# Optimization experiments

Measured on AMD Instinct MI355X. Metric: run time of the kernel, lower is better.

Reference implementation:

```python
import jax, jax.numpy as jnp
import numpy as np

B, N_IN, N_HID, T = 64, 512, 512, 512


def setup_inputs() -> dict:
    key = jax.random.key(0)
    k1, k2, k3, k4, k5 = jax.random.split(key, 5)
    scale = 1.0 / np.sqrt(N_HID).astype(np.float32)
    return {
        "X": jax.random.normal(k1, (B, N_IN, T), dtype=jnp.float32),
        "Wax": jax.random.normal(k2, (N_IN, N_HID), dtype=jnp.float32) * scale,
        "Waa": jax.random.normal(k3, (N_HID, N_HID), dtype=jnp.float32) * scale,
        "bx": jax.random.normal(k4, (N_HID,), dtype=jnp.float32) * scale,
        "ba": jax.random.normal(k5, (N_HID,), dtype=jnp.float32) * scale,
    }


def reference(X, Wax, Waa, bx, ba):
    # X: [B, n_in, T]. a_{t+1} = tanh(x_t @ Wax + bx + a_t @ Waa + ba)
    # Precompute the input projections for all timesteps in one big GEMM:
    # [T, B, n_hid]
    Xt = jnp.transpose(X, (2, 0, 1))  # [T, B, n_in]
    inp_proj = jnp.einsum('tbi,ih->tbh', Xt, Wax) + bx + ba

    def step(a, u):
        a_next = jnp.tanh(u + a @ Waa)
        return a_next, a_next

    a0 = jnp.zeros((X.shape[0], Waa.shape[0]), dtype=X.dtype)
    _, A = jax.lax.scan(step, a0, inp_proj)
    return A  # [T, B, n_hid] == stacked A[1:] of the torch module
```

## Files before the change

kernel.cpp:

```cpp
#include <hip/hip_runtime.h>
#include <math.h>

#define BB   64
#define NIN  512
#define NH   512
#define TT   512

typedef _Float16 half2_t __attribute__((ext_vector_type(2)));
typedef _Float16 half8_t __attribute__((ext_vector_type(8)));
typedef float    f32x4  __attribute__((ext_vector_type(4)));

__device__ __forceinline__ unsigned pk16(float x, float y) {
    unsigned lo = (unsigned)__builtin_bit_cast(unsigned short, (_Float16)x);
    unsigned hi = (unsigned)__builtin_bit_cast(unsigned short, (_Float16)y);
    return lo | (hi << 16);
}

__device__ __forceinline__ float dot2u(unsigned w, unsigned a, float acc) {
    return __builtin_amdgcn_fdot2(__builtin_bit_cast(half2_t, w),
                                  __builtin_bit_cast(half2_t, a), acc, false);
}

__device__ __forceinline__ float tanh_fast(float x) {
    float ax = __builtin_fabsf(x);
    float e  = __builtin_amdgcn_exp2f(-2.885390082f * ax);
    float r  = (1.0f - e) * __builtin_amdgcn_rcpf(1.0f + e);
    return __builtin_copysignf(r, x);
}

#define NX4 (BB * (NIN / 2) * (TT / 4))
#define NW4 ((NIN / 2) * (NH / 4))

__global__ __launch_bounds__(256) void pack_f16(
    const float* __restrict__ X, const float* __restrict__ Wax,
    unsigned* __restrict__ Xp, unsigned* __restrict__ Wp)
{
    const int gid = blockIdx.x * 256 + threadIdx.x;
    if (gid < NX4) {
        const int t4 = gid & (TT / 4 - 1);
        const int pr = gid >> 7;
        const int j  = pr & (NIN / 2 - 1);
        const int b  = pr >> 8;
        float4 r0 = *(const float4*)&X[((size_t)b * NIN + 2 * j    ) * TT + t4 * 4];
        float4 r1 = *(const float4*)&X[((size_t)b * NIN + 2 * j + 1) * TT + t4 * 4];
        uint4 o;
        o.x = pk16(r0.x, r1.x); o.y = pk16(r0.y, r1.y);
        o.z = pk16(r0.z, r1.z); o.w = pk16(r0.w, r1.w);
        *(uint4*)&Xp[(size_t)pr * TT + t4 * 4] = o;
    } else {
        const int g = gid - NX4;
        if (g < NW4) {
            const int h4 = g & (NH / 4 - 1);
            const int j  = g >> 7;
            float4 r0 = *(const float4*)&Wax[((size_t)(2 * j    )) * NH + h4 * 4];
            float4 r1 = *(const float4*)&Wax[((size_t)(2 * j + 1)) * NH + h4 * 4];
            uint4 o;
            o.x = pk16(r0.x, r1.x); o.y = pk16(r0.y, r1.y);
            o.z = pk16(r0.z, r1.z); o.w = pk16(r0.w, r1.w);
            *(uint4*)&Wp[(size_t)j * NH + h4 * 4] = o;
        }
    }
}

__global__ __launch_bounds__(256) void inp_proj_mfma_pk(
    const unsigned* __restrict__ Xp, const unsigned* __restrict__ Wp,
    const float* __restrict__ bx, const float* __restrict__ ba,
    float* __restrict__ out)
{
    __shared__ unsigned Xsp[16][132];
    __shared__ unsigned Wsp[16][132];

    const int b   = blockIdx.z;
    const int t0  = blockIdx.y * 128;
    const int h0  = blockIdx.x * 128;
    const int tid = threadIdx.x;
    const int lane = tid & 63;
    const int wid  = tid >> 6;
    const int wm   = wid >> 1;
    const int wn   = wid & 1;
    const int q    = lane >> 4;
    const int r16  = lane & 15;

    const int lr = tid >> 4;
    const int lc = (tid & 15) * 8;

    const unsigned* Xb = Xp + (size_t)b * (NIN / 2) * TT;

    f32x4 acc[4][4] = {};

    for (int p0 = 0; p0 < NIN / 2; p0 += 16) {
        const unsigned* Arow = &Xb[(size_t)(p0 + lr) * TT + t0 + lc];
        const unsigned* Brow = &Wp[(size_t)(p0 + lr) * NH + h0 + lc];
        uint4 xa = *(const uint4*)&Arow[0];
        uint4 xb = *(const uint4*)&Arow[4];
        uint4 wa = *(const uint4*)&Brow[0];
        uint4 wb = *(const uint4*)&Brow[4];

        __syncthreads();
        *(uint4*)&Xsp[lr][lc]     = xa;
        *(uint4*)&Xsp[lr][lc + 4] = xb;
        *(uint4*)&Wsp[lr][lc]     = wa;
        *(uint4*)&Wsp[lr][lc + 4] = wb;
        __syncthreads();

        uint4 af[4], bf[4];
#pragma unroll
        for (int mt = 0; mt < 4; ++mt) {
            const int tc = wm * 64 + mt * 16 + r16;
            af[mt].x = Xsp[4 * q + 0][tc];
            af[mt].y = Xsp[4 * q + 1][tc];
            af[mt].z = Xsp[4 * q + 2][tc];
            af[mt].w = Xsp[4 * q + 3][tc];
        }
#pragma unroll
        for (int nt = 0; nt < 4; ++nt) {
            const int hc = wn * 64 + nt * 16 + r16;
            bf[nt].x = Wsp[4 * q + 0][hc];
            bf[nt].y = Wsp[4 * q + 1][hc];
            bf[nt].z = Wsp[4 * q + 2][hc];
            bf[nt].w = Wsp[4 * q + 3][hc];
        }
#pragma unroll
        for (int mt = 0; mt < 4; ++mt)
#pragma unroll
            for (int nt = 0; nt < 4; ++nt)
                acc[mt][nt] = __builtin_amdgcn_mfma_f32_16x16x32_f16(
                    __builtin_bit_cast(half8_t, af[mt]),
                    __builtin_bit_cast(half8_t, bf[nt]),
                    acc[mt][nt], 0, 0, 0);
    }

#pragma unroll
    for (int nt = 0; nt < 4; ++nt) {
        const int h = h0 + wn * 64 + nt * 16 + r16;
        const float bias = bx[h] + ba[h];
#pragma unroll
        for (int mt = 0; mt < 4; ++mt) {
            const int trow = t0 + wm * 64 + mt * 16 + q * 4;
#pragma unroll
            for (int rr = 0; rr < 4; ++rr) {
                out[(size_t)(trow + rr) * (BB * NH) + (size_t)b * NH + h] =
                    acc[mt][nt][rr] + bias;
            }
        }
    }
}

__global__ __launch_bounds__(256) void inp_proj_mfma(
    const float* __restrict__ X, const float* __restrict__ Wax,
    const float* __restrict__ bx, const float* __restrict__ ba,
    float* __restrict__ out)
{
    __shared__ unsigned Xsp[16][132];
    __shared__ unsigned Wsp[16][132];

    const int b   = blockIdx.z;
    const int t0  = blockIdx.y * 128;
    const int h0  = blockIdx.x * 128;
    const int tid = threadIdx.x;
    const int lane = tid & 63;
    const int wid  = tid >> 6;
    const int wm   = wid >> 1;
    const int wn   = wid & 1;
    const int q    = lane >> 4;
    const int r16  = lane & 15;

    const int lr = tid >> 4;
    const int lc = (tid & 15) * 8;

    const float* Xb = X + (size_t)b * NIN * TT;

    f32x4 acc[4][4] = {};

    for (int i0 = 0; i0 < NIN; i0 += 32) {
        const int k0 = i0 + 2 * lr, k1 = k0 + 1;
        float4 xa0 = *(const float4*)&Xb[(size_t)k0 * TT + t0 + lc];
        float4 xa1 = *(const float4*)&Xb[(size_t)k0 * TT + t0 + lc + 4];
        float4 xb0 = *(const float4*)&Xb[(size_t)k1 * TT + t0 + lc];
        float4 xb1 = *(const float4*)&Xb[(size_t)k1 * TT + t0 + lc + 4];
        float4 wa0 = *(const float4*)&Wax[(size_t)k0 * NH + h0 + lc];
        float4 wa1 = *(const float4*)&Wax[(size_t)k0 * NH + h0 + lc + 4];
        float4 wb0 = *(const float4*)&Wax[(size_t)k1 * NH + h0 + lc];
        float4 wb1 = *(const float4*)&Wax[(size_t)k1 * NH + h0 + lc + 4];

        uint4 xp0, xp1, wp0, wp1;
        xp0.x = pk16(xa0.x, xb0.x); xp0.y = pk16(xa0.y, xb0.y);
        xp0.z = pk16(xa0.z, xb0.z); xp0.w = pk16(xa0.w, xb0.w);
        xp1.x = pk16(xa1.x, xb1.x); xp1.y = pk16(xa1.y, xb1.y);
        xp1.z = pk16(xa1.z, xb1.z); xp1.w = pk16(xa1.w, xb1.w);
        wp0.x = pk16(wa0.x, wb0.x); wp0.y = pk16(wa0.y, wb0.y);
        wp0.z = pk16(wa0.z, wb0.z); wp0.w = pk16(wa0.w, wb0.w);
        wp1.x = pk16(wa1.x, wb1.x); wp1.y = pk16(wa1.y, wb1.y);
        wp1.z = pk16(wa1.z, wb1.z); wp1.w = pk16(wa1.w, wb1.w);

        __syncthreads();
        *(uint4*)&Xsp[lr][lc]     = xp0;
        *(uint4*)&Xsp[lr][lc + 4] = xp1;
        *(uint4*)&Wsp[lr][lc]     = wp0;
        *(uint4*)&Wsp[lr][lc + 4] = wp1;
        __syncthreads();

        uint4 af[4], bf[4];
#pragma unroll
        for (int mt = 0; mt < 4; ++mt) {
            const int tc = wm * 64 + mt * 16 + r16;
            af[mt].x = Xsp[4 * q + 0][tc];
            af[mt].y = Xsp[4 * q + 1][tc];
            af[mt].z = Xsp[4 * q + 2][tc];
            af[mt].w = Xsp[4 * q + 3][tc];
        }
#pragma unroll
        for (int nt = 0; nt < 4; ++nt) {
            const int hc = wn * 64 + nt * 16 + r16;
            bf[nt].x = Wsp[4 * q + 0][hc];
            bf[nt].y = Wsp[4 * q + 1][hc];
            bf[nt].z = Wsp[4 * q + 2][hc];
            bf[nt].w = Wsp[4 * q + 3][hc];
        }
#pragma unroll
        for (int mt = 0; mt < 4; ++mt)
#pragma unroll
            for (int nt = 0; nt < 4; ++nt)
                acc[mt][nt] = __builtin_amdgcn_mfma_f32_16x16x32_f16(
                    __builtin_bit_cast(half8_t, af[mt]),
                    __builtin_bit_cast(half8_t, bf[nt]),
                    acc[mt][nt], 0, 0, 0);
    }

#pragma unroll
    for (int nt = 0; nt < 4; ++nt) {
        const int h = h0 + wn * 64 + nt * 16 + r16;
        const float bias = bx[h] + ba[h];
#pragma unroll
        for (int mt = 0; mt < 4; ++mt) {
            const int trow = t0 + wm * 64 + mt * 16 + q * 4;
#pragma unroll
            for (int rr = 0; rr < 4; ++rr) {
                out[(size_t)(trow + rr) * (BB * NH) + (size_t)b * NH + h] =
                    acc[mt][nt][rr] + bias;
            }
        }
    }
}

#define NRP 24
#define NLP 8
#define PSTRIDE 516

__device__ __forceinline__ unsigned bline(unsigned a, int l) {
    return (unsigned)__builtin_amdgcn_readlane((int)a, l);
}

__global__ __launch_bounds__(1024, 4) void rnn_scan_v6(
    const float* __restrict__ Waa, float* __restrict__ out)
{
    __shared__ uint4    wldsv[NLP][1024];
    __shared__ unsigned a_lds[2][256];
    __shared__ float    part[8][PSTRIDE];

    const int tid  = threadIdx.x;
    const int b    = blockIdx.x;
    const int cidx = tid & 127;
    const int kq   = tid >> 7;
    const int h4   = cidx * 4;
    const int l32  = tid & 31;

    unsigned w0[NRP], w1[NRP], w2[NRP], w3[NRP];
#pragma unroll
    for (int j = 0; j < NRP; ++j) {
        const int k = kq * 64 + 2 * j;
        float4 r0 = *(const float4*)&Waa[(size_t)k       * NH + h4];
        float4 r1 = *(const float4*)&Waa[(size_t)(k + 1) * NH + h4];
        w0[j] = pk16(r0.x, r1.x);
        w1[j] = pk16(r0.y, r1.y);
        w2[j] = pk16(r0.z, r1.z);
        w3[j] = pk16(r0.w, r1.w);
    }
#pragma unroll
    for (int p = 0; p < NLP; ++p) {
        const int k = kq * 64 + 2 * (NRP + p);
        float4 r0 = *(const float4*)&Waa[(size_t)k       * NH + h4];
        float4 r1 = *(const float4*)&Waa[(size_t)(k + 1) * NH + h4];
        uint4 wv;
        wv.x = pk16(r0.x, r1.x);
        wv.y = pk16(r0.y, r1.y);
        wv.z = pk16(r0.z, r1.z);
        wv.w = pk16(r0.w, r1.w);
        wldsv[p][tid] = wv;
    }

    if (tid < 256) a_lds[0][tid] = 0u;
    __syncthreads();

    const int  hc  = tid & 511;
    const bool red = (tid < 512);
    float* ob = out + (size_t)b * NH + hc;
    float u_cur = red ? ob[0] : 0.0f;

    for (int t = 0; t < TT; ++t) {
        const int tn = (t + 1 < TT) ? (t + 1) : (TT - 1);
        float u_next = red ? ob[(size_t)tn * (BB * NH)] : 0.0f;

        unsigned a_loc = a_lds[t & 1][kq * 32 + l32];

        float acc0 = 0.f, acc1 = 0.f, acc2 = 0.f, acc3 = 0.f;
#pragma unroll
        for (int j = 0; j < NRP; j += 2) {
            unsigned ra = bline(a_loc, j);
            unsigned rb = bline(a_loc, j + 1);
            acc0 = dot2u(w0[j], ra, acc0);
            acc1 = dot2u(w1[j], ra, acc1);
            acc2 = dot2u(w2[j], ra, acc2);
            acc3 = dot2u(w3[j], ra, acc3);
            acc0 = dot2u(w0[j + 1], rb, acc0);
            acc1 = dot2u(w1[j + 1], rb, acc1);
            acc2 = dot2u(w2[j + 1], rb, acc2);
            acc3 = dot2u(w3[j + 1], rb, acc3);
        }
#pragma unroll
        for (int p = 0; p < NLP; ++p) {
            unsigned ra = bline(a_loc, NRP + p);
            uint4 v = wldsv[p][tid];
            acc0 = dot2u(v.x, ra, acc0);
            acc1 = dot2u(v.y, ra, acc1);
            acc2 = dot2u(v.z, ra, acc2);
            acc3 = dot2u(v.w, ra, acc3);
        }

        float4 pv; pv.x = acc0; pv.y = acc1; pv.z = acc2; pv.w = acc3;
        *(float4*)&part[kq][h4] = pv;
        __builtin_amdgcn_s_waitcnt(0xC07F);
        __builtin_amdgcn_s_barrier();

        if (red) {
            float x = u_cur +
                (((part[0][hc] + part[1][hc]) + (part[2][hc] + part[3][hc])) +
                 ((part[4][hc] + part[5][hc]) + (part[6][hc] + part[7][hc])));
            float an = tanh_fast(x);
            ob[(size_t)t * (BB * NH)] = an;
            ((unsigned short*)a_lds[(t + 1) & 1])[hc] =
                __builtin_bit_cast(unsigned short, (_Float16)an);
        }
        u_cur = u_next;
        __builtin_amdgcn_s_waitcnt(0xC07F);
        __builtin_amdgcn_s_barrier();
    }
}

extern "C" void kernel_launch(void* const* d_in, const int* in_sizes, int n_in,
                              void* d_out, int out_size, void* d_ws, size_t ws_size,
                              hipStream_t stream) {
    const float* X   = (const float*)d_in[0];
    const float* Wax = (const float*)d_in[1];
    const float* Waa = (const float*)d_in[2];
    const float* bx  = (const float*)d_in[3];
    const float* ba  = (const float*)d_in[4];
    float* out = (float*)d_out;

    const size_t xp_dw = (size_t)BB * (NIN / 2) * TT;
    const size_t wp_dw = (size_t)(NIN / 2) * NH;
    const size_t need  = (xp_dw + wp_dw) * sizeof(unsigned);

    if (ws_size >= need) {
        unsigned* Xp = (unsigned*)d_ws;
        unsigned* Wp = Xp + xp_dw;
        const int npack = (NX4 + NW4 + 255) / 256;
        pack_f16<<<npack, 256, 0, stream>>>(X, Wax, Xp, Wp);
        dim3 g1(NH / 128, TT / 128, BB);
        inp_proj_mfma_pk<<<g1, 256, 0, stream>>>(Xp, Wp, bx, ba, out);
    } else {
        dim3 g1(NH / 128, TT / 128, BB);
        inp_proj_mfma<<<g1, 256, 0, stream>>>(X, Wax, bx, ba, out);
    }
    rnn_scan_v6<<<BB, 1024, 0, stream>>>(Waa, out);
}
```

Baseline: 965.2 us.

## Reduce RNN step partials via LDS atomics and drop second barrier

```diff
diff --git a/kernel.cpp b/kernel.cpp
--- a/kernel.cpp
+++ b/kernel.cpp
@@ -245,63 +245,65 @@
 
 #define NRP 24
 #define NLP 8
-#define PSTRIDE 516
 
 __device__ __forceinline__ unsigned bline(unsigned a, int l) {
     return (unsigned)__builtin_amdgcn_readlane((int)a, l);
 }
 
-__global__ __launch_bounds__(1024, 4) void rnn_scan_v6(
+__global__ __launch_bounds__(1024, 4) void rnn_scan_v8(
     const float* __restrict__ Waa, float* __restrict__ out)
 {
-    __shared__ uint4    wldsv[NLP][1024];
-    __shared__ unsigned a_lds[2][256];
-    __shared__ float    part[8][PSTRIDE];
+    __shared__ uint4 wldsv[NLP][1024];
+    __shared__ float part[3][512];
 
     const int tid  = threadIdx.x;
     const int b    = blockIdx.x;
     const int cidx = tid & 127;
     const int kq   = tid >> 7;
-    const int h4   = cidx * 4;
     const int l32  = tid & 31;
+    const int wv   = tid >> 6;
 
     unsigned w0[NRP], w1[NRP], w2[NRP], w3[NRP];
 #pragma unroll
     for (int j = 0; j < NRP; ++j) {
         const int k = kq * 64 + 2 * j;
-        float4 r0 = *(const float4*)&Waa[(size_t)k       * NH + h4];
-        float4 r1 = *(const float4*)&Waa[(size_t)(k + 1) * NH + h4];
-        w0[j] = pk16(r0.x, r1.x);
-        w1[j] = pk16(r0.y, r1.y);
-        w2[j] = pk16(r0.z, r1.z);
-        w3[j] = pk16(r0.w, r1.w);
+        const float* r0 = &Waa[(size_t)k * NH + cidx];
+        const float* r1 = &Waa[(size_t)(k + 1) * NH + cidx];
+        w0[j] = pk16(r0[0],   r1[0]);
+        w1[j] = pk16(r0[128], r1[128]);
+        w2[j] = pk16(r0[256], r1[256]);
+        w3[j] = pk16(r0[384], r1[384]);
     }
 #pragma unroll
     for (int p = 0; p < NLP; ++p) {
         const int k = kq * 64 + 2 * (NRP + p);
-        float4 r0 = *(const float4*)&Waa[(size_t)k       * NH + h4];
-        float4 r1 = *(const float4*)&Waa[(size_t)(k + 1) * NH + h4];
-        uint4 wv;
-        wv.x = pk16(r0.x, r1.x);
-        wv.y = pk16(r0.y, r1.y);
-        wv.z = pk16(r0.z, r1.z);
-        wv.w = pk16(r0.w, r1.w);
-        wldsv[p][tid] = wv;
-    }
-
-    if (tid < 256) a_lds[0][tid] = 0u;
+        const float* r0 = &Waa[(size_t)k * NH + cidx];
+        const float* r1 = &Waa[(size_t)(k + 1) * NH + cidx];
+        uint4 wvv;
+        wvv.x = pk16(r0[0],   r1[0]);
+        wvv.y = pk16(r0[128], r1[128]);
+        wvv.z = pk16(r0[256], r1[256]);
+        wvv.w = pk16(r0[384], r1[384]);
+        wldsv[p][tid] = wvv;
+    }
+
+    if (tid < 512) {
+        part[0][tid] = 0.0f;
+        part[1][tid] = 0.0f;
+        part[2][tid] = 0.0f;
+    }
     __syncthreads();
 
-    const int  hc  = tid & 511;
-    const bool red = (tid < 512);
-    float* ob = out + (size_t)b * NH + hc;
-    float u_cur = red ? ob[0] : 0.0f;
-
+    const int h2 = kq * 64 + 2 * l32;
+    const float* ub = out + (size_t)b * NH + h2;
+    float2 u_cur = *(const float2*)ub;
+    unsigned a_loc = 0u;
+    const bool gate = ((tid & 32) == 0) && ((wv & 1) == 0);
+
+    int pb = 0;
     for (int t = 0; t < TT; ++t) {
         const int tn = (t + 1 < TT) ? (t + 1) : (TT - 1);
-        float u_next = red ? ob[(size_t)tn * (BB * NH)] : 0.0f;
-
-        unsigned a_loc = a_lds[t & 1][kq * 32 + l32];
+        float2 u_next = *(const float2*)&ub[(size_t)tn * (BB * NH)];
 
         float acc0 = 0.f, acc1 = 0.f, acc2 = 0.f, acc3 = 0.f;
 #pragma unroll
@@ -327,23 +329,28 @@
             acc3 = dot2u(v.w, ra, acc3);
         }
 
-        float4 pv; pv.x = acc0; pv.y = acc1; pv.z = acc2; pv.w = acc3;
-        *(float4*)&part[kq][h4] = pv;
+        atomicAdd(&part[pb][cidx      ], acc0);
+        atomicAdd(&part[pb][cidx + 128], acc1);
+        atomicAdd(&part[pb][cidx + 256], acc2);
+        atomicAdd(&part[pb][cidx + 384], acc3);
         __builtin_amdgcn_s_waitcnt(0xC07F);
         __builtin_amdgcn_s_barrier();
 
-        if (red) {
-            float x = u_cur +
-                (((part[0][hc] + part[1][hc]) + (part[2][hc] + part[3][hc])) +
-                 ((part[4][hc] + part[5][hc]) + (part[6][hc] + part[7][hc])));
-            float an = tanh_fast(x);
-            ob[(size_t)t * (BB * NH)] = an;
-            ((unsigned short*)a_lds[(t + 1) & 1])[hc] =
-                __builtin_bit_cast(unsigned short, (_Float16)an);
-        }
+        float2 s = *(const float2*)&part[pb][h2];
+        const int zb = (pb >= 1) ? (pb - 1) : 2;
+        if (gate) {
+            float2 z; z.x = 0.0f; z.y = 0.0f;
+            *(float2*)&part[zb][h2] = z;
+        }
+        float an0 = tanh_fast(u_cur.x + s.x);
+        float an1 = tanh_fast(u_cur.y + s.y);
+        if (gate) {
+            float2 st; st.x = an0; st.y = an1;
+            *(float2*)&out[(size_t)t * (BB * NH) + (size_t)b * NH + h2] = st;
+        }
+        a_loc = pk16(an0, an1);
         u_cur = u_next;
-        __builtin_amdgcn_s_waitcnt(0xC07F);
-        __builtin_amdgcn_s_barrier();
+        pb = (pb == 2) ? 0 : (pb + 1);
     }
 }
 
@@ -372,5 +379,5 @@
         dim3 g1(NH / 128, TT / 128, BB);
         inp_proj_mfma<<<g1, 256, 0, stream>>>(X, Wax, bx, ba, out);
     }
-    rnn_scan_v6<<<BB, 1024, 0, stream>>>(Waa, out);
-}
+    rnn_scan_v8<<<BB, 1024, 0, stream>>>(Waa, out);
+}
```

Measured after the change: 3.246 ms. 236% more time.

## Use MFMA with broadcast hidden state in recurrent scan, drop partial-sum reduction

Applied to the files above, without the earlier changes.

```diff
diff --git a/kernel.cpp b/kernel.cpp
--- a/kernel.cpp
+++ b/kernel.cpp
@@ -14,11 +14,6 @@
     unsigned lo = (unsigned)__builtin_bit_cast(unsigned short, (_Float16)x);
     unsigned hi = (unsigned)__builtin_bit_cast(unsigned short, (_Float16)y);
     return lo | (hi << 16);
-}
-
-__device__ __forceinline__ float dot2u(unsigned w, unsigned a, float acc) {
-    return __builtin_amdgcn_fdot2(__builtin_bit_cast(half2_t, w),
-                                  __builtin_bit_cast(half2_t, a), acc, false);
 }
 
 __device__ __forceinline__ float tanh_fast(float x) {
@@ -243,105 +238,99 @@
     }
 }
 
-#define NRP 24
-#define NLP 8
-#define PSTRIDE 516
-
-__device__ __forceinline__ unsigned bline(unsigned a, int l) {
-    return (unsigned)__builtin_amdgcn_readlane((int)a, l);
-}
-
-__global__ __launch_bounds__(1024, 4) void rnn_scan_v6(
+#define RKT 12
+#define LKT 4
+
+__global__ __launch_bounds__(1024, 4) void rnn_scan_v9(
     const float* __restrict__ Waa, float* __restrict__ out)
 {
-    __shared__ uint4    wldsv[NLP][1024];
-    __shared__ unsigned a_lds[2][256];
-    __shared__ float    part[8][PSTRIDE];
-
-    const int tid  = threadIdx.x;
-    const int b    = blockIdx.x;
-    const int cidx = tid & 127;
-    const int kq   = tid >> 7;
-    const int h4   = cidx * 4;
-    const int l32  = tid & 31;
-
-    unsigned w0[NRP], w1[NRP], w2[NRP], w3[NRP];
-#pragma unroll
-    for (int j = 0; j < NRP; ++j) {
-        const int k = kq * 64 + 2 * j;
-        float4 r0 = *(const float4*)&Waa[(size_t)k       * NH + h4];
-        float4 r1 = *(const float4*)&Waa[(size_t)(k + 1) * NH + h4];
-        w0[j] = pk16(r0.x, r1.x);
-        w1[j] = pk16(r0.y, r1.y);
-        w2[j] = pk16(r0.z, r1.z);
-        w3[j] = pk16(r0.w, r1.w);
-    }
-#pragma unroll
-    for (int p = 0; p < NLP; ++p) {
-        const int k = kq * 64 + 2 * (NRP + p);
-        float4 r0 = *(const float4*)&Waa[(size_t)k       * NH + h4];
-        float4 r1 = *(const float4*)&Waa[(size_t)(k + 1) * NH + h4];
-        uint4 wv;
-        wv.x = pk16(r0.x, r1.x);
-        wv.y = pk16(r0.y, r1.y);
-        wv.z = pk16(r0.z, r1.z);
-        wv.w = pk16(r0.w, r1.w);
-        wldsv[p][tid] = wv;
-    }
-
-    if (tid < 256) a_lds[0][tid] = 0u;
+    __shared__ uint4 wlds[LKT * 2][1024];
+    __shared__ unsigned short a_h[2][NH];
+
+    const int tid = threadIdx.x;
+    const int b   = blockIdx.x;
+    const int w   = tid >> 6;
+    const int l   = tid & 63;
+    const int q   = l >> 4;
+    const int c0  = w * 32 + (l & 15);
+    const int c1  = c0 + 16;
+
+    uint4 br0[RKT], br1[RKT];
+#pragma unroll
+    for (int kk = 0; kk < RKT; ++kk) {
+        const int kb = kk * 32 + 8 * q;
+        uint4 v0, v1;
+        v0.x = pk16(Waa[(size_t)(kb + 0) * NH + c0], Waa[(size_t)(kb + 1) * NH + c0]);
+        v0.y = pk16(Waa[(size_t)(kb + 2) * NH + c0], Waa[(size_t)(kb + 3) * NH + c0]);
+        v0.z = pk16(Waa[(size_t)(kb + 4) * NH + c0], Waa[(size_t)(kb + 5) * NH + c0]);
+        v0.w = pk16(Waa[(size_t)(kb + 6) * NH + c0], Waa[(size_t)(kb + 7) * NH + c0]);
+        v1.x = pk16(Waa[(size_t)(kb + 0) * NH + c1], Waa[(size_t)(kb + 1) * NH + c1]);
+        v1.y = pk16(Waa[(size_t)(kb + 2) * NH + c1], Waa[(size_t)(kb + 3) * NH + c1]);
+        v1.z = pk16(Waa[(size_t)(kb + 4) * NH + c1], Waa[(size_t)(kb + 5) * NH + c1]);
+        v1.w = pk16(Waa[(size_t)(kb + 6) * NH + c1], Waa[(size_t)(kb + 7) * NH + c1]);
+        br0[kk] = v0;
+        br1[kk] = v1;
+    }
+#pragma unroll
+    for (int kk = 0; kk < LKT; ++kk) {
+        const int kb = (RKT + kk) * 32 + 8 * q;
+        uint4 v0, v1;
+        v0.x = pk16(Waa[(size_t)(kb + 0) * NH + c0], Waa[(size_t)(kb + 1) * NH + c0]);
+        v0.y = pk16(Waa[(size_t)(kb + 2) * NH + c0], Waa[(size_t)(kb + 3) * NH + c0]);
+        v0.z = pk16(Waa[(size_t)(kb + 4) * NH + c0], Waa[(size_t)(kb + 5) * NH + c0]);
+        v0.w = pk16(Waa[(size_t)(kb + 6) * NH + c0], Waa[(size_t)(kb + 7) * NH + c0]);
+        v1.x = pk16(Waa[(size_t)(kb + 0) * NH + c1], Waa[(size_t)(kb + 1) * NH + c1]);
+        v1.y = pk16(Waa[(size_t)(kb + 2) * NH + c1], Waa[(size_t)(kb + 3) * NH + c1]);
+        v1.z = pk16(Waa[(size_t)(kb + 4) * NH + c1], Waa[(size_t)(kb + 5) * NH + c1]);
+        v1.w = pk16(Waa[(size_t)(kb + 6) * NH + c1], Waa[(size_t)(kb + 7) * NH + c1]);
+        wlds[kk * 2 + 0][tid] = v0;
+        wlds[kk * 2 + 1][tid] = v1;
+    }
+
+    if (tid < 256) *(unsigned*)&a_h[0][tid * 2] = 0u;
     __syncthreads();
 
-    const int  hc  = tid & 511;
-    const bool red = (tid < 512);
-    float* ob = out + (size_t)b * NH + hc;
-    float u_cur = red ? ob[0] : 0.0f;
+    const float* ub0 = out + (size_t)b * NH + c0;
+    const float* ub1 = out + (size_t)b * NH + c1;
+    float u0 = ub0[0], u1 = ub1[0];
 
     for (int t = 0; t < TT; ++t) {
         const int tn = (t + 1 < TT) ? (t + 1) : (TT - 1);
-        float u_next = red ? ob[(size_t)tn * (BB * NH)] : 0.0f;
-
-        unsigned a_loc = a_lds[t & 1][kq * 32 + l32];
-
-        float acc0 = 0.f, acc1 = 0.f, acc2 = 0.f, acc3 = 0.f;
-#pragma unroll
-        for (int j = 0; j < NRP; j += 2) {
-            unsigned ra = bline(a_loc, j);
-            unsigned rb = bline(a_loc, j + 1);
-            acc0 = dot2u(w0[j], ra, acc0);
-            acc1 = dot2u(w1[j], ra, acc1);
-            acc2 = dot2u(w2[j], ra, acc2);
-            acc3 = dot2u(w3[j], ra, acc3);
-            acc0 = dot2u(w0[j + 1], rb, acc0);
-            acc1 = dot2u(w1[j + 1], rb, acc1);
-            acc2 = dot2u(w2[j + 1], rb, acc2);
-            acc3 = dot2u(w3[j + 1], rb, acc3);
-        }
-#pragma unroll
-        for (int p = 0; p < NLP; ++p) {
-            unsigned ra = bline(a_loc, NRP + p);
-            uint4 v = wldsv[p][tid];
-            acc0 = dot2u(v.x, ra, acc0);
-            acc1 = dot2u(v.y, ra, acc1);
-            acc2 = dot2u(v.z, ra, acc2);
-            acc3 = dot2u(v.w, ra, acc3);
-        }
-
-        float4 pv; pv.x = acc0; pv.y = acc1; pv.z = acc2; pv.w = acc3;
-        *(float4*)&part[kq][h4] = pv;
-        __builtin_amdgcn_s_waitcnt(0xC07F);
-        __builtin_amdgcn_s_barrier();
-
-        if (red) {
-            float x = u_cur +
-                (((part[0][hc] + part[1][hc]) + (part[2][hc] + part[3][hc])) +
-                 ((part[4][hc] + part[5][hc]) + (part[6][hc] + part[7][hc])));
-            float an = tanh_fast(x);
-            ob[(size_t)t * (BB * NH)] = an;
-            ((unsigned short*)a_lds[(t + 1) & 1])[hc] =
-                __builtin_bit_cast(unsigned short, (_Float16)an);
-        }
-        u_cur = u_next;
+        float un0 = ub0[(size_t)tn * (BB * NH)];
+        float un1 = ub1[(size_t)tn * (BB * NH)];
+
+        const unsigned short* ac = a_h[t & 1];
+        f32x4 acc0 = {}, acc1 = {};
+#pragma unroll
+        for (int kk = 0; kk < 16; ++kk) {
+            uint4 av = *(const uint4*)&ac[kk * 32 + q * 8];
+            half8_t A = __builtin_bit_cast(half8_t, av);
+            uint4 b0, b1;
+            if (kk < RKT) {
+                b0 = br0[kk];
+                b1 = br1[kk];
+            } else {
+                b0 = wlds[(kk - RKT) * 2 + 0][tid];
+                b1 = wlds[(kk - RKT) * 2 + 1][tid];
+            }
+            acc0 = __builtin_amdgcn_mfma_f32_16x16x32_f16(
+                A, __builtin_bit_cast(half8_t, b0), acc0, 0, 0, 0);
+            acc1 = __builtin_amdgcn_mfma_f32_16x16x32_f16(
+                A, __builtin_bit_cast(half8_t, b1), acc1, 0, 0, 0);
+        }
+
+        float an0 = tanh_fast(u0 + acc0[0]);
+        float an1 = tanh_fast(u1 + acc1[0]);
+
+        unsigned short* an = a_h[(t + 1) & 1];
+        if (l < 16) {
+            an[c0] = __builtin_bit_cast(unsigned short, (_Float16)an0);
+            an[c1] = __builtin_bit_cast(unsigned short, (_Float16)an1);
+            out[(size_t)t * (BB * NH) + (size_t)b * NH + c0] = an0;
+            out[(size_t)t * (BB * NH) + (size_t)b * NH + c1] = an1;
+        }
+        u0 = un0;
+        u1 = un1;
         __builtin_amdgcn_s_waitcnt(0xC07F);
         __builtin_amdgcn_s_barrier();
     }
@@ -372,5 +361,5 @@
         dim3 g1(NH / 128, TT / 128, BB);
         inp_proj_mfma<<<g1, 256, 0, stream>>>(X, Wax, bx, ba, out);
     }
-    rnn_scan_v6<<<BB, 1024, 0, stream>>>(Waa, out);
-}
+    rnn_scan_v9<<<BB, 1024, 0, stream>>>(Waa, out);
+}
```

New measurement: 920.9 us. 1.05x faster.
